# Kernel optimization log

Measured on AMD Instinct MI355X. Metric: run time of the kernel, lower is better.

Reference implementation:

```python
import jax, jax.numpy as jnp
import numpy as np

B, H, S, D = 4, 16, 4096, 64

def setup_inputs() -> dict:
    key = jax.random.key(0)
    kq, kk, kv = jax.random.split(key, 3)
    q = jax.random.normal(kq, (B, H, S, D), dtype=jnp.float32)
    k = jax.random.normal(kk, (B, H, S, D), dtype=jnp.float32)
    v = jax.random.normal(kv, (B, H, S, D), dtype=jnp.float32)
    return {"q": q, "k": k, "v": v}

def reference(q, k, v):
    # Original: (q @ k^T) @ v with score [B,H,S,S].
    # Mathematically identical reassociation: q @ (k^T @ v),
    # state kv has shape [B,H,D,D] -> avoids the SxS intermediate.
    kv = jnp.einsum('bhsd,bhse->bhde', k, v)  # [B,H,D,D]
    out = jnp.einsum('bhsd,bhde->bhse', q, kv)  # [B,H,S,D]
    return out
```

## Files before the change

kernel.cpp:

```cpp
#include <hip/hip_runtime.h>

#define BH  64
#define SEQ 4096
#define DH  64
#define NCHUNK 16
#define CROWS  (SEQ / NCHUNK)
#define NT     (CROWS / 32)

typedef __attribute__((ext_vector_type(8))) short bf16x8v;
typedef __attribute__((ext_vector_type(4))) float f32x4v;

__device__ __forceinline__ short f2bf(float x) {
  unsigned u = __float_as_uint(x);
  return (short)((u + 0x7FFFu + ((u >> 16) & 1u)) >> 16);
}

__device__ __forceinline__ void gload_lds16(const float* g, float* l) {
  __builtin_amdgcn_global_load_lds(
      (const __attribute__((address_space(1))) void*)g,
      (__attribute__((address_space(3))) void*)l, 16, 0, 0);
}

__global__ __launch_bounds__(256, 4) void kv_partial_kernel(
    const float* __restrict__ k, const float* __restrict__ v,
    float* __restrict__ partial) {
  const int t = threadIdx.x;
  const int bh = blockIdx.x >> 4;
  const int chunk = blockIdx.x & (NCHUNK - 1);

  const int l  = t & 63;
  const int w  = t >> 6;
  const int lg = l >> 4;
  const int ln = l & 15;
  const int d0 = (w & 1) * 32;
  const int e0 = (w >> 1) * 32;

  const float* kb = k + (size_t)bh * SEQ * DH + (size_t)chunk * CROWS * DH;
  const float* vb = v + (size_t)bh * SEQ * DH + (size_t)chunk * CROWS * DH;

  __shared__ float smem[8192];

  auto STAGE = [&](int tt) {
    const int buf = tt & 1;
    const size_t goff = (size_t)tt * 32 * DH;
    const int wo = w * 256;
#pragma unroll
    for (int i = 0; i < 2; ++i) {
      gload_lds16(kb + goff + i * 1024 + wo + l * 4,
                  smem + buf * 2048 + i * 1024 + wo);
      gload_lds16(vb + goff + i * 1024 + wo + l * 4,
                  smem + 4096 + buf * 2048 + i * 1024 + wo);
    }
  };

  f32x4v acc00 = {0.f, 0.f, 0.f, 0.f};
  f32x4v acc01 = acc00, acc10 = acc00, acc11 = acc00;

  STAGE(0);
  asm volatile("s_waitcnt vmcnt(0)" ::: "memory");
  __syncthreads();

  for (int tt = 0; tt < NT; ++tt) {
    if (tt + 1 < NT) STAGE(tt + 1);

    const float* ksb = smem + (tt & 1) * 2048;
    const float* vsb = smem + 4096 + (tt & 1) * 2048;

    bf16x8v a0, a1, b0, b1;
#pragma unroll
    for (int j = 0; j < 8; ++j) {
      const int r = (lg * 8 + j) * 64;
      a0[j] = f2bf(ksb[r + d0 + ln]);
      a1[j] = f2bf(ksb[r + d0 + 16 + ln]);
      b0[j] = f2bf(vsb[r + e0 + ln]);
      b1[j] = f2bf(vsb[r + e0 + 16 + ln]);
    }

    acc00 = __builtin_amdgcn_mfma_f32_16x16x32_bf16(a0, b0, acc00, 0, 0, 0);
    acc01 = __builtin_amdgcn_mfma_f32_16x16x32_bf16(a0, b1, acc01, 0, 0, 0);
    acc10 = __builtin_amdgcn_mfma_f32_16x16x32_bf16(a1, b0, acc10, 0, 0, 0);
    acc11 = __builtin_amdgcn_mfma_f32_16x16x32_bf16(a1, b1, acc11, 0, 0, 0);

    asm volatile("s_waitcnt vmcnt(0)" ::: "memory");
    __syncthreads();
  }

  float* pb = partial + (size_t)blockIdx.x * (DH * DH);
  const int rbase = lg * 4;
#pragma unroll
  for (int r = 0; r < 4; ++r) {
    pb[(d0 +  0 + rbase + r) * 64 + e0 +  0 + ln] = acc00[r];
    pb[(d0 +  0 + rbase + r) * 64 + e0 + 16 + ln] = acc01[r];
    pb[(d0 + 16 + rbase + r) * 64 + e0 +  0 + ln] = acc10[r];
    pb[(d0 + 16 + rbase + r) * 64 + e0 + 16 + ln] = acc11[r];
  }
}

__global__ __launch_bounds__(256) void kv_reduce_kernel(
    const float* __restrict__ partial, float* __restrict__ kvf) {
  const int gid = blockIdx.x * 256 + threadIdx.x;
  const int bh = gid >> 10;
  const int idx = gid & 1023;
  float4 s = {0.f, 0.f, 0.f, 0.f};
  for (int c = 0; c < NCHUNK; ++c) {
    const float4* p = (const float4*)(partial + ((size_t)bh * NCHUNK + c) * (DH * DH));
    float4 x = p[idx];
    s.x += x.x; s.y += x.y; s.z += x.z; s.w += x.w;
  }
  ((float4*)kvf)[gid] = s;
}

__global__ __launch_bounds__(256) void out_kernel(
    const float* __restrict__ q, const float* __restrict__ kvf,
    float* __restrict__ out) {
  const int t = threadIdx.x;
  const int bh = blockIdx.x >> 6;
  const int rb = blockIdx.x & 63;
  const int row = rb * 64 + (t >> 2);
  const int c0 = (t & 3) * 16;

  __shared__ float kv_lds[64 * 64];

  const float4* gkv4 = (const float4*)(kvf + (size_t)bh * (DH * DH));
  float4* kv4 = (float4*)kv_lds;
#pragma unroll
  for (int j = 0; j < 4; ++j) kv4[t + j * 256] = gkv4[t + j * 256];

  const float* qrow = q + (size_t)bh * SEQ * DH + (size_t)row * DH;
  float4 qv[16];
#pragma unroll
  for (int i = 0; i < 16; ++i) qv[i] = *(const float4*)&qrow[i * 4];

  __syncthreads();

  float acc[16];
#pragma unroll
  for (int j = 0; j < 16; ++j) acc[j] = 0.f;

#pragma unroll
  for (int dc = 0; dc < 16; ++dc) {
    float qs[4] = {qv[dc].x, qv[dc].y, qv[dc].z, qv[dc].w};
#pragma unroll
    for (int dd = 0; dd < 4; ++dd) {
      const float* kr = &kv_lds[(dc * 4 + dd) * 64 + c0];
      float4 k0 = *(const float4*)&kr[0];
      float4 k1 = *(const float4*)&kr[4];
      float4 k2 = *(const float4*)&kr[8];
      float4 k3 = *(const float4*)&kr[12];
      const float qsv = qs[dd];
      acc[0]  += qsv * k0.x; acc[1]  += qsv * k0.y;
      acc[2]  += qsv * k0.z; acc[3]  += qsv * k0.w;
      acc[4]  += qsv * k1.x; acc[5]  += qsv * k1.y;
      acc[6]  += qsv * k1.z; acc[7]  += qsv * k1.w;
      acc[8]  += qsv * k2.x; acc[9]  += qsv * k2.y;
      acc[10] += qsv * k2.z; acc[11] += qsv * k2.w;
      acc[12] += qsv * k3.x; acc[13] += qsv * k3.y;
      acc[14] += qsv * k3.z; acc[15] += qsv * k3.w;
    }
  }

  float* ob = out + (size_t)bh * SEQ * DH + (size_t)row * DH + c0;
#pragma unroll
  for (int j = 0; j < 4; ++j) {
    float4 w = {acc[4 * j + 0], acc[4 * j + 1], acc[4 * j + 2], acc[4 * j + 3]};
    *(float4*)&ob[4 * j] = w;
  }
}

extern "C" void kernel_launch(void* const* d_in, const int* in_sizes, int n_in,
                              void* d_out, int out_size, void* d_ws, size_t ws_size,
                              hipStream_t stream) {
  const float* q = (const float*)d_in[0];
  const float* k = (const float*)d_in[1];
  const float* v = (const float*)d_in[2];
  float* out = (float*)d_out;

  float* kvf = (float*)d_ws;
  float* partial = kvf + (size_t)BH * DH * DH;

  hipLaunchKernelGGL(kv_partial_kernel, dim3(BH * NCHUNK), dim3(256), 0, stream,
                     k, v, partial);
  hipLaunchKernelGGL(kv_reduce_kernel, dim3(256), dim3(256), 0, stream,
                     partial, kvf);
  hipLaunchKernelGGL(out_kernel, dim3(BH * 64), dim3(256), 0, stream,
                     q, kvf, out);
}
```

Before: 76.91 us.

## Restructure kv partial kernel to single-wave blocks with swizzled LDS and deeper prefetch

Rewrites the K^T V partial kernel so each block is a single 64-thread wave computing the full 64x64 tile with a 4x4 grid of MFMA accumulators. The sequence is split into twice as many chunks. LDS loads are XOR-swizzled to reduce bank conflicts, and a two-stage prefetch with partial vmcnt waits replaces the full wait and __syncthreads per step. In exchange it doubles the partial-buffer traffic and the reduce work, and it relies on the swizzle and vmcnt counts being correct.

```diff
diff --git a/kernel.cpp b/kernel.cpp
--- a/kernel.cpp
+++ b/kernel.cpp
@@ -3,7 +3,7 @@
 #define BH  64
 #define SEQ 4096
 #define DH  64
-#define NCHUNK 16
+#define NCHUNK 32
 #define CROWS  (SEQ / NCHUNK)
 #define NT     (CROWS / 32)
 
@@ -21,79 +21,84 @@
       (__attribute__((address_space(3))) void*)l, 16, 0, 0);
 }
 
-__global__ __launch_bounds__(256, 4) void kv_partial_kernel(
+__global__ __launch_bounds__(64) void kv_partial_kernel(
     const float* __restrict__ k, const float* __restrict__ v,
     float* __restrict__ partial) {
-  const int t = threadIdx.x;
-  const int bh = blockIdx.x >> 4;
+  const int l  = threadIdx.x;
+  const int bh = blockIdx.x >> 5;
   const int chunk = blockIdx.x & (NCHUNK - 1);
-
-  const int l  = t & 63;
-  const int w  = t >> 6;
   const int lg = l >> 4;
   const int ln = l & 15;
-  const int d0 = (w & 1) * 32;
-  const int e0 = (w >> 1) * 32;
 
   const float* kb = k + (size_t)bh * SEQ * DH + (size_t)chunk * CROWS * DH;
   const float* vb = v + (size_t)bh * SEQ * DH + (size_t)chunk * CROWS * DH;
 
   __shared__ float smem[8192];
 
+  f32x4v acc[4][4];
+#pragma unroll
+  for (int m = 0; m < 4; ++m)
+#pragma unroll
+    for (int n = 0; n < 4; ++n) acc[m][n] = (f32x4v){0.f, 0.f, 0.f, 0.f};
+
   auto STAGE = [&](int tt) {
     const int buf = tt & 1;
-    const size_t goff = (size_t)tt * 32 * DH;
-    const int wo = w * 256;
+    const float* kt = kb + (size_t)tt * 2048;
+    const float* vt = vb + (size_t)tt * 2048;
+    float* kd = smem + buf * 2048;
+    float* vd = smem + 4096 + buf * 2048;
 #pragma unroll
-    for (int i = 0; i < 2; ++i) {
-      gload_lds16(kb + goff + i * 1024 + wo + l * 4,
-                  smem + buf * 2048 + i * 1024 + wo);
-      gload_lds16(vb + goff + i * 1024 + wo + l * 4,
-                  smem + 4096 + buf * 2048 + i * 1024 + wo);
+    for (int i = 0; i < 8; ++i) {
+      const int so = (i * 4 + lg) * 64 + ((ln * 4) ^ (((i >> 1) & 3) << 4));
+      gload_lds16(kt + so, kd + i * 256);
+      gload_lds16(vt + so, vd + i * 256);
     }
   };
 
-  f32x4v acc00 = {0.f, 0.f, 0.f, 0.f};
-  f32x4v acc01 = acc00, acc10 = acc00, acc11 = acc00;
+  auto COMPUTE = [&](int tt) {
+    const float* ks = smem + (tt & 1) * 2048;
+    const float* vs = smem + 4096 + (tt & 1) * 2048;
+    bf16x8v a[4], b[4];
+#pragma unroll
+    for (int c = 0; c < 4; ++c) {
+#pragma unroll
+      for (int j = 0; j < 8; ++j) {
+        const int addr = (lg * 8 + j) * 64 + ((c * 16 + ln) ^ (lg << 4));
+        a[c][j] = f2bf(ks[addr]);
+        b[c][j] = f2bf(vs[addr]);
+      }
+    }
+#pragma unroll
+    for (int m = 0; m < 4; ++m)
+#pragma unroll
+      for (int n = 0; n < 4; ++n)
+        acc[m][n] = __builtin_amdgcn_mfma_f32_16x16x32_bf16(
+            a[m], b[n], acc[m][n], 0, 0, 0);
+  };
 
   STAGE(0);
-  asm volatile("s_waitcnt vmcnt(0)" ::: "memory");
-  __syncthreads();
-
+  STAGE(1);
+#pragma unroll
   for (int tt = 0; tt < NT; ++tt) {
-    if (tt + 1 < NT) STAGE(tt + 1);
-
-    const float* ksb = smem + (tt & 1) * 2048;
-    const float* vsb = smem + 4096 + (tt & 1) * 2048;
-
-    bf16x8v a0, a1, b0, b1;
-#pragma unroll
-    for (int j = 0; j < 8; ++j) {
-      const int r = (lg * 8 + j) * 64;
-      a0[j] = f2bf(ksb[r + d0 + ln]);
-      a1[j] = f2bf(ksb[r + d0 + 16 + ln]);
-      b0[j] = f2bf(vsb[r + e0 + ln]);
-      b1[j] = f2bf(vsb[r + e0 + 16 + ln]);
+    if (tt + 1 < NT) {
+      asm volatile("s_waitcnt vmcnt(16)" ::: "memory");
+    } else {
+      asm volatile("s_waitcnt vmcnt(0)" ::: "memory");
     }
-
-    acc00 = __builtin_amdgcn_mfma_f32_16x16x32_bf16(a0, b0, acc00, 0, 0, 0);
-    acc01 = __builtin_amdgcn_mfma_f32_16x16x32_bf16(a0, b1, acc01, 0, 0, 0);
-    acc10 = __builtin_amdgcn_mfma_f32_16x16x32_bf16(a1, b0, acc10, 0, 0, 0);
-    acc11 = __builtin_amdgcn_mfma_f32_16x16x32_bf16(a1, b1, acc11, 0, 0, 0);
-
-    asm volatile("s_waitcnt vmcnt(0)" ::: "memory");
-    __syncthreads();
+    __builtin_amdgcn_sched_barrier(0);
+    COMPUTE(tt);
+    __builtin_amdgcn_sched_barrier(0);
+    if (tt + 2 < NT) STAGE(tt + 2);
   }
 
   float* pb = partial + (size_t)blockIdx.x * (DH * DH);
-  const int rbase = lg * 4;
 #pragma unroll
-  for (int r = 0; r < 4; ++r) {
-    pb[(d0 +  0 + rbase + r) * 64 + e0 +  0 + ln] = acc00[r];
-    pb[(d0 +  0 + rbase + r) * 64 + e0 + 16 + ln] = acc01[r];
-    pb[(d0 + 16 + rbase + r) * 64 + e0 +  0 + ln] = acc10[r];
-    pb[(d0 + 16 + rbase + r) * 64 + e0 + 16 + ln] = acc11[r];
-  }
+  for (int m = 0; m < 4; ++m)
+#pragma unroll
+    for (int n = 0; n < 4; ++n)
+#pragma unroll
+      for (int r = 0; r < 4; ++r)
+        pb[(m * 16 + lg * 4 + r) * 64 + n * 16 + ln] = acc[m][n][r];
 }
 
 __global__ __launch_bounds__(256) void kv_reduce_kernel(
@@ -178,7 +183,7 @@
   float* kvf = (float*)d_ws;
   float* partial = kvf + (size_t)BH * DH * DH;
 
-  hipLaunchKernelGGL(kv_partial_kernel, dim3(BH * NCHUNK), dim3(256), 0, stream,
+  hipLaunchKernelGGL(kv_partial_kernel, dim3(BH * NCHUNK), dim3(64), 0, stream,
                      k, v, partial);
   hipLaunchKernelGGL(kv_reduce_kernel, dim3(256), dim3(256), 0, stream,
                      partial, kvf);
```

Measured after the change: 82.92 us. +7.8%, slower.
